# Performance work log

Measured on AMD Instinct MI355X. Metric: run time of the kernel, lower is better.

Reference implementation:

```python
import jax, jax.numpy as jnp
import numpy as np

N = 50000      # nodes
E = 800000     # edges (before self-loops)
IN_CH = 5
HID = 32
HEADS = 4
NEG_SLOPE = 0.2  # PyG GATConv default


def _gat_layer(x, src, dst, W, att_src, att_dst, bias, concat):
    """PyG GATConv (eval mode). W: [F_in, H*C], att_*: [H, C], bias matches output."""
    H, C = att_src.shape
    h = (x @ W).reshape(-1, H, C)                       # [N, H, C]
    a_src = jnp.sum(h * att_src, axis=-1)               # [N, H]
    a_dst = jnp.sum(h * att_dst, axis=-1)               # [N, H]
    e = jax.nn.leaky_relu(a_src[src] + a_dst[dst], negative_slope=NEG_SLOPE)  # [E', H]
    m = jax.ops.segment_max(e, dst, num_segments=N)     # stable softmax per dst segment
    ex = jnp.exp(e - m[dst])
    denom = jax.ops.segment_sum(ex, dst, num_segments=N)
    alpha = ex / denom[dst]                             # [E', H]
    out = jax.ops.segment_sum(alpha[:, :, None] * h[src], dst, num_segments=N)  # [N, H, C]
    out = out.reshape(N, H * C) if concat else out.mean(axis=1)
    return out + bias


def setup_inputs() -> dict:
    key = jax.random.key(0)
    ks = jax.random.split(key, 14)
    g = lambda k, shape, s=0.1: (jax.random.normal(k, shape, jnp.float32) * s)
    return {
        "x": jax.random.normal(ks[0], (N, IN_CH), jnp.float32),
        "edge_index": jax.random.randint(ks[1], (2, E), 0, N, jnp.int32),
        "W1": g(ks[2], (IN_CH, HEADS * HID)),
        "att_src1": g(ks[3], (HEADS, HID)),
        "att_dst1": g(ks[4], (HEADS, HID)),
        "b1": jnp.zeros((HEADS * HID,), jnp.float32),
        "W2": g(ks[5], (HEADS * HID, HID)),
        "att_src2": g(ks[6], (1, HID)),
        "att_dst2": g(ks[7], (1, HID)),
        "b2": jnp.zeros((HID,), jnp.float32),
        "Wc1": g(ks[8], (HID, 16)),
        "bc1": jnp.zeros((16,), jnp.float32),
        "Wc2": g(ks[9], (16, 1)),
        "bc2": jnp.zeros((1,), jnp.float32),
    }


def reference(x, edge_index, W1, att_src1, att_dst1, b1, W2, att_src2, att_dst2, b2, Wc1, bc1, Wc2, bc2):
    # add self loops (PyG GATConv default add_self_loops=True)
    loops = jnp.arange(N, dtype=edge_index.dtype)
    src = jnp.concatenate([edge_index[0], loops])
    dst = jnp.concatenate([edge_index[1], loops])
    # dropout layers are identity in eval mode
    h = jax.nn.elu(_gat_layer(x, src, dst, W1, att_src1, att_dst1, b1, concat=True))
    h = jax.nn.elu(_gat_layer(h, src, dst, W2, att_src2, att_dst2, b2, concat=False))
    h = jax.nn.relu(h @ Wc1 + bc1)
    out = (h @ Wc2 + bc2)[:, 0]   # squeeze(-1) -> [N]
    return out
```

## Files before the change

kernel.cpp:

```cpp
#include <hip/hip_runtime.h>
#include <hip/hip_fp16.h>

#define NEG_SLOPE 0.2f
#define BSHIFT 6
#define SCATB 256

__device__ __forceinline__ float elu1(float v) { return v > 0.f ? v : expm1f(v); }
__device__ __forceinline__ float lrelu(float v) { return v > 0.f ? v : NEG_SLOPE * v; }

__device__ __forceinline__ int ge_off(const int* __restrict__ blkoff,
                                      const int* __restrict__ bsum2, int j) {
    if (j == 0) return 0;
    int b = (j - 1) >> 8;
    int v = blkoff[j];
    if (b >= 1) v += bsum2[b - 1];
    return v;
}


__global__ __launch_bounds__(256) void k_cnt_attn(
    const int* __restrict__ ei, int E, int ET, int chunk,
    int* __restrict__ Cmat, int nbuck,
    const float* __restrict__ x, const float* __restrict__ W1,
    const float* __restrict__ att_s, const float* __restrict__ att_d,
    float* __restrict__ rec, int N) {
    __shared__ int hist[784];
    __shared__ float Ps[5][4], Pd[5][4];
    if (blockIdx.x < SCATB) {
        for (int i = threadIdx.x; i < nbuck; i += 256) hist[i] = 0;
        __syncthreads();
        int k = blockIdx.x;
        int e0 = k * chunk, e1 = min(e0 + chunk, ET);
        for (int e = e0 + threadIdx.x; e < e1; e += 256) {
            int d = (e < E) ? ei[E + e] : e - E;
            atomicAdd(&hist[d >> BSHIFT], 1);
        }
        __syncthreads();
        for (int i = threadIdx.x; i < nbuck; i += 256)
            Cmat[i * SCATB + k] = hist[i];
    } else {
        if (threadIdx.x < 40) {
            int pair = threadIdx.x & 1, idx = threadIdx.x >> 1;
            int k = idx >> 2, h = idx & 3;
            const float* att = pair ? att_d : att_s;
            float r = 0.f;
#pragma unroll
            for (int c = 0; c < 32; ++c) r = fmaf(W1[k * 128 + h * 32 + c], att[h * 32 + c], r);
            if (pair) Pd[k][h] = r; else Ps[k][h] = r;
        }
        __syncthreads();
        int n = (blockIdx.x - SCATB) * 256 + threadIdx.x;
        if (n >= N) return;
        float xv[5];
#pragma unroll
        for (int k = 0; k < 5; ++k) xv[k] = x[(size_t)n * 5 + k];
        float s0 = 0, s1 = 0, s2 = 0, s3 = 0, d0 = 0, d1 = 0, d2 = 0, d3 = 0;
#pragma unroll
        for (int k = 0; k < 5; ++k) {
            s0 = fmaf(xv[k], Ps[k][0], s0); s1 = fmaf(xv[k], Ps[k][1], s1);
            s2 = fmaf(xv[k], Ps[k][2], s2); s3 = fmaf(xv[k], Ps[k][3], s3);
            d0 = fmaf(xv[k], Pd[k][0], d0); d1 = fmaf(xv[k], Pd[k][1], d1);
            d2 = fmaf(xv[k], Pd[k][2], d2); d3 = fmaf(xv[k], Pd[k][3], d3);
        }
        float* r = rec + (size_t)n * 16;
        *(float4*)(r)      = make_float4(s0, s1, s2, s3);
        *(float4*)(r + 4)  = make_float4(xv[0], xv[1], xv[2], xv[3]);
        r[8] = xv[4];
        *(float4*)(r + 12) = make_float4(d0, d1, d2, d3);
    }
}

__global__ __launch_bounds__(256) void k_scan1(
    const int* __restrict__ Cmat, int* __restrict__ blkoff, int* __restrict__ bsum, int M) {
    __shared__ int ws4[4], wsoff[4];
    int i = blockIdx.x * 256 + threadIdx.x;
    int lane = threadIdx.x & 63, w = threadIdx.x >> 6;
    int v = (i < M) ? Cmat[i] : 0;
    int sc = v;
#pragma unroll
    for (int m = 1; m < 64; m <<= 1) {
        int t = __shfl_up(sc, m, 64);
        if (lane >= m) sc += t;
    }
    if (lane == 63) ws4[w] = sc;
    __syncthreads();
    if (threadIdx.x == 0) {
        int r = 0;
#pragma unroll
        for (int j = 0; j < 4; ++j) { wsoff[j] = r; r += ws4[j]; }
        bsum[blockIdx.x] = r;
    }
    __syncthreads();
    if (i < M) blkoff[i + 1] = sc + wsoff[w];
}

__global__ __launch_bounds__(1024) void k_scan2(
    int* __restrict__ bsum, int nb, int* __restrict__ off, int N, int ET) {
    __shared__ int wsum[16];
    int i = threadIdx.x, lane = i & 63, w = i >> 6;
    if (i == 0) off[N] = ET;
    int v = (i < nb) ? bsum[i] : 0, sc = v;
#pragma unroll
    for (int m = 1; m < 64; m <<= 1) {
        int t = __shfl_up(sc, m, 64);
        if (lane >= m) sc += t;
    }
    if (lane == 63) wsum[w] = sc;
    __syncthreads();
    if (w == 0 && lane < 16) {
        int s2 = wsum[lane];
#pragma unroll
        for (int m = 1; m < 16; m <<= 1) {
            int t = __shfl_up(s2, m, 16);
            if (lane >= m) s2 += t;
        }
        wsum[lane] = s2;
    }
    __syncthreads();
    int carry = (w == 0) ? 0 : wsum[w - 1];
    if (i < nb) bsum[i] = carry + sc;
}

__global__ __launch_bounds__(256) void k_scat(
    const int* __restrict__ ei, int E, int ET, int chunk,
    const int* __restrict__ blkoff, const int* __restrict__ bsum2,
    unsigned* __restrict__ pairs, int nbuck) {
    __shared__ int cur[784];
    int k = blockIdx.x;
    for (int i = threadIdx.x; i < nbuck; i += 256)
        cur[i] = ge_off(blkoff, bsum2, i * SCATB + k);
    __syncthreads();
    int e0 = k * chunk, e1 = min(e0 + chunk, ET);
    for (int e = e0 + threadIdx.x; e < e1; e += 256) {
        int s, d;
        if (e < E) { s = ei[e]; d = ei[E + e]; } else { s = d = e - E; }
        int p = atomicAdd(&cur[d >> BSHIFT], 1);
        pairs[p] = (unsigned)s | ((unsigned)(d & 63) << 16);
    }
}

__global__ __launch_bounds__(256) void k_sortB(
    const unsigned* __restrict__ pairs, const int* __restrict__ blkoff,
    const int* __restrict__ bsum2, int* __restrict__ off,
    int* __restrict__ csr_src, int N, int ET, int nbuck) {
    __shared__ int hist[64], cur[64];
    __shared__ unsigned pl[1536];
    int b = blockIdx.x;
    int base = ge_off(blkoff, bsum2, b * SCATB);
    int end  = (b + 1 < nbuck) ? ge_off(blkoff, bsum2, (b + 1) * SCATB) : ET;
    int cnt = end - base;
    int stg = min(cnt, 1536);
    int dstBase = b << BSHIFT;
    if (threadIdx.x < 64) hist[threadIdx.x] = 0;
    for (int i = threadIdx.x; i < stg; i += 256) pl[i] = pairs[base + i];
    __syncthreads();
    for (int i = threadIdx.x; i < cnt; i += 256) {
        unsigned pr = (i < stg) ? pl[i] : pairs[base + i];
        atomicAdd(&hist[pr >> 16], 1);
    }
    __syncthreads();
    if (threadIdx.x < 64) {
        int v = hist[threadIdx.x], sc = v;
#pragma unroll
        for (int m = 1; m < 64; m <<= 1) {
            int t = __shfl_up(sc, m, 64);
            if (threadIdx.x >= m) sc += t;
        }
        int ex = sc - v;
        cur[threadIdx.x] = ex;
        int d = dstBase + threadIdx.x;
        if (d < N) off[d] = base + ex;
    }
    __syncthreads();
    for (int i = threadIdx.x; i < cnt; i += 256) {
        unsigned pr = (i < stg) ? pl[i] : pairs[base + i];
        int r = atomicAdd(&cur[pr >> 16], 1);
        csr_src[base + r] = (int)(pr & 0xFFFFu);
    }
}


__global__ __launch_bounds__(256) void k_agg1(
    const int* __restrict__ off, const int* __restrict__ csr_src,
    const float* __restrict__ rec, const float* __restrict__ W1,
    const float* __restrict__ b1, __half* __restrict__ out1h, int N) {
    __shared__ float Wl[5 * 128];
    __shared__ float b1l[128];
    for (int i = threadIdx.x; i < 5 * 128; i += 256) Wl[i] = W1[i];
    if (threadIdx.x < 128) b1l[threadIdx.x] = b1[threadIdx.x];
    __syncthreads();
    int g = (blockIdx.x * 256 + threadIdx.x) >> 4;
    int lane = threadIdx.x & 15;
    if (g >= N) return;
    int p0 = off[g], p1 = off[g + 1];
    float4 ad = *(const float4*)(rec + (size_t)g * 16 + 12);
    float den0 = 0, den1 = 0, den2 = 0, den3 = 0;
    float acc[4][5] = {};
    for (int p = p0 + lane; p < p1; p += 16) {
        int s = csr_src[p];
        const float* r = rec + (size_t)s * 16;
        float4 as  = *(const float4*)r;
        float4 x03 = *(const float4*)(r + 4);
        float  x4  = r[8];
        float v0 = __expf(lrelu(as.x + ad.x));
        float v1 = __expf(lrelu(as.y + ad.y));
        float v2 = __expf(lrelu(as.z + ad.z));
        float v3 = __expf(lrelu(as.w + ad.w));
        den0 += v0; den1 += v1; den2 += v2; den3 += v3;
        float xk[5] = {x03.x, x03.y, x03.z, x03.w, x4};
#pragma unroll
        for (int k = 0; k < 5; ++k) {
            acc[0][k] = fmaf(v0, xk[k], acc[0][k]);
            acc[1][k] = fmaf(v1, xk[k], acc[1][k]);
            acc[2][k] = fmaf(v2, xk[k], acc[2][k]);
            acc[3][k] = fmaf(v3, xk[k], acc[3][k]);
        }
    }
#pragma unroll
    for (int m = 8; m; m >>= 1) {
        den0 += __shfl_xor(den0, m, 16); den1 += __shfl_xor(den1, m, 16);
        den2 += __shfl_xor(den2, m, 16); den3 += __shfl_xor(den3, m, 16);
#pragma unroll
        for (int h = 0; h < 4; ++h)
#pragma unroll
            for (int k = 0; k < 5; ++k) acc[h][k] += __shfl_xor(acc[h][k], m, 16);
    }
    int c0 = lane * 8;
    int h = lane >> 2;
    float dh = (h == 0) ? den0 : (h == 1) ? den1 : (h == 2) ? den2 : den3;
    float ih = 1.f / dh;
    float ag[5];
#pragma unroll
    for (int k = 0; k < 5; ++k) ag[k] = acc[h][k] * ih;
    __half2 ph[4];
#pragma unroll
    for (int j = 0; j < 4; ++j) {
        int c = c0 + 2 * j;
        float rr = b1l[c];
#pragma unroll
        for (int k = 0; k < 5; ++k) rr = fmaf(ag[k], Wl[k * 128 + c], rr);
        float oa = elu1(rr);
        rr = b1l[c + 1];
#pragma unroll
        for (int k = 0; k < 5; ++k) rr = fmaf(ag[k], Wl[k * 128 + c + 1], rr);
        float ob = elu1(rr);
        ph[j] = __floats2half2_rn(oa, ob);
    }
    *(float4*)(out1h + (size_t)g * 128 + c0) = *(float4*)ph;
}


__global__ __launch_bounds__(256) void k_feat2(
    const __half* __restrict__ out1h, const float* __restrict__ W2,
    const float* __restrict__ att_s, const float* __restrict__ att_d,
    __half* __restrict__ h2h, float* __restrict__ a_s, float* __restrict__ a_d, int N) {
    __shared__ float Wl[128 * 32];
    for (int i = threadIdx.x; i < 128 * 32; i += 256) Wl[i] = W2[i];
    __syncthreads();
    int t = blockIdx.x * 256 + threadIdx.x;
    int n = t >> 5, c = t & 31;
    if (n >= N) return;
    const float4* hr4 = (const float4*)(out1h + (size_t)n * 128);
    float acc = 0.f;
#pragma unroll
    for (int k4 = 0; k4 < 16; ++k4) {
        float4 q = hr4[k4];
        const __half2* hp = (const __half2*)&q;
#pragma unroll
        for (int m = 0; m < 4; ++m) {
            float2 f = __half22float2(hp[m]);
            acc = fmaf(f.x, Wl[(k4 * 8 + 2 * m) * 32 + c], acc);
            acc = fmaf(f.y, Wl[(k4 * 8 + 2 * m + 1) * 32 + c], acc);
        }
    }
    h2h[(size_t)n * 32 + c] = __float2half_rn(acc);
    float as = acc * att_s[c], ad = acc * att_d[c];
#pragma unroll
    for (int m = 16; m; m >>= 1) {
        as += __shfl_xor(as, m, 32);
        ad += __shfl_xor(ad, m, 32);
    }
    if (c == 0) { a_s[n] = as; a_d[n] = ad; }
}

__global__ __launch_bounds__(256) void k_agg2h(
    const int* __restrict__ off, const int* __restrict__ csr_src,
    const float* __restrict__ a_s, const float* __restrict__ a_d,
    const __half* __restrict__ h2h, const float* __restrict__ b2,
    const float* __restrict__ Wc1, const float* __restrict__ bc1,
    const float* __restrict__ Wc2, const float* __restrict__ bc2,
    float* __restrict__ out, int N) {
    __shared__ float Wl[512];
    __shared__ float b2l[32], b1l[16], w2l[16];
    for (int i = threadIdx.x; i < 512; i += 256) Wl[i] = Wc1[i];
    if (threadIdx.x < 32) b2l[threadIdx.x] = b2[threadIdx.x];
    if (threadIdx.x < 16) {
        b1l[threadIdx.x] = bc1[threadIdx.x];
        w2l[threadIdx.x] = Wc2[threadIdx.x];
    }
    __syncthreads();
    int g = (blockIdx.x * 256 + threadIdx.x) >> 5;
    int lane = threadIdx.x & 31;
    if (g >= N) return;
    int p0 = off[g], p1 = off[g + 1];
    float ad = a_d[g];
    float acc = 0.f, den = 0.f;
    for (int base = p0; base < p1; base += 32) {
        int rem = p1 - base;
        int s = g;
        float w = 0.f;
        if (lane < rem) {
            s = csr_src[base + lane];
            w = __expf(lrelu(a_s[s] + ad));
        }
        den += w;
        int cnt = min(rem, 32);
        int rc = (cnt + 7) & ~7;
        for (int j = 0; j < rc; j += 8) {
#pragma unroll
            for (int jj = 0; jj < 8; ++jj) {
                int   sj = __shfl(s, j + jj, 32);
                float wj = __shfl(w, j + jj, 32);
                float hv = __half2float(h2h[(size_t)sj * 32 + lane]);
                acc = fmaf(wj, hv, acc);
            }
        }
    }
#pragma unroll
    for (int m = 16; m; m >>= 1) den += __shfl_xor(den, m, 32);
    float z = elu1(fmaf(acc, 1.f / den, b2l[lane]));
    float y = b1l[lane & 15];
#pragma unroll
    for (int c = 0; c < 32; ++c) {
        float zc = __shfl(z, c, 32);
        y = fmaf(zc, Wl[c * 16 + (lane & 15)], y);
    }
    y = fmaxf(y, 0.f);
    float t = (lane < 16) ? y * w2l[lane] : 0.f;
#pragma unroll
    for (int m = 8; m; m >>= 1) t += __shfl_xor(t, m, 32);
    if (lane == 0) out[g] = t + bc2[0];
}

extern "C" void kernel_launch(void* const* d_in, const int* in_sizes, int n_in,
                              void* d_out, int out_size, void* d_ws, size_t ws_size,
                              hipStream_t stream) {
    const float* x   = (const float*)d_in[0];
    const int*   ei  = (const int*)d_in[1];
    const float* W1  = (const float*)d_in[2];
    const float* as1 = (const float*)d_in[3];
    const float* ad1 = (const float*)d_in[4];
    const float* b1  = (const float*)d_in[5];
    const float* W2  = (const float*)d_in[6];
    const float* as2 = (const float*)d_in[7];
    const float* ad2 = (const float*)d_in[8];
    const float* b2  = (const float*)d_in[9];
    const float* Wc1 = (const float*)d_in[10];
    const float* bc1 = (const float*)d_in[11];
    const float* Wc2 = (const float*)d_in[12];
    const float* bc2 = (const float*)d_in[13];
    float* out = (float*)d_out;

    const int N = out_size;
    const int E = in_sizes[1] / 2;
    const int ET = E + N;
    const int nbuck = (N + 63) >> BSHIFT;
    const int M = nbuck * SCATB;
    const int chunk = (ET + SCATB - 1) / SCATB;

    float*    ws    = (float*)d_ws;
    __half*   out1h = (__half*)ws;
    __half*   h2h   = (__half*)(ws + (size_t)N * 64);
    float*    rec   = ws + (size_t)N * 80;
    float*    a_s2  = rec  + (size_t)N * 16;
    float*    a_d2  = a_s2 + N;
    int*      off   = (int*)(a_d2 + N);
    int*      csr_src = off + (N + 2);
    int*      Cmat  = csr_src + ET;
    int*      blkoff = Cmat + M;
    int*      bsum  = blkoff + (M + 2);
    unsigned* pairs = (unsigned*)(bsum + 1024);

    auto cdiv = [](long long a, long long b) { return (int)((a + b - 1) / b); };
    const int B = 256;
    const int NB2 = cdiv(M, B);
    const int nAttn = cdiv(N, B);

    k_cnt_attn<<<SCATB + nAttn, B, 0, stream>>>(ei, E, ET, chunk, Cmat, nbuck,
                                                x, W1, as1, ad1, rec, N);
    k_scan1<<<NB2, B, 0, stream>>>(Cmat, blkoff, bsum, M);
    k_scan2<<<1, 1024, 0, stream>>>(bsum, NB2, off, N, ET);
    k_scat<<<SCATB, B, 0, stream>>>(ei, E, ET, chunk, blkoff, bsum, pairs, nbuck);
    k_sortB<<<nbuck, B, 0, stream>>>(pairs, blkoff, bsum, off, csr_src, N, ET, nbuck);

    k_agg1<<<cdiv((long long)N * 16, B), B, 0, stream>>>(off, csr_src, rec, W1, b1, out1h, N);

    k_feat2<<<cdiv((long long)N * 32, B), B, 0, stream>>>(out1h, W2, as2, ad2, h2h, a_s2, a_d2, N);
    k_agg2h<<<cdiv((long long)N * 32, B), B, 0, stream>>>(off, csr_src, a_s2, a_d2, h2h, b2,
                                                          Wc1, bc1, Wc2, bc2, out, N);
}
```

Baseline: 117.6 us.

## Single-pass decoupled-lookback scan, fp16 node records, transposed fp16 W2 in LDS

Replaces the two-kernel scan (block scan plus a single-block carry scan) with one decoupled-lookback scan that uses a ticket counter and per-block descriptors. The descriptors are zeroed inside the first kernel, which also makes blkoff fully global so consumers no longer add the carry. Layer-1 node records are packed as fp16 (32 B) and a_dst is moved to a separate float4 array, cutting gather bytes in agg1. k_feat2 stores W2 transposed in fp16 in LDS so each thread reads contiguous half2 weights. These changes trade one launch for spin-wait risk and add fp16 rounding of the attention logits and input features.

```diff
diff --git a/kernel.cpp b/kernel.cpp
--- a/kernel.cpp
+++ b/kernel.cpp
@@ -7,15 +7,6 @@
 
 __device__ __forceinline__ float elu1(float v) { return v > 0.f ? v : expm1f(v); }
 __device__ __forceinline__ float lrelu(float v) { return v > 0.f ? v : NEG_SLOPE * v; }
-
-__device__ __forceinline__ int ge_off(const int* __restrict__ blkoff,
-                                      const int* __restrict__ bsum2, int j) {
-    if (j == 0) return 0;
-    int b = (j - 1) >> 8;
-    int v = blkoff[j];
-    if (b >= 1) v += bsum2[b - 1];
-    return v;
-}
 
 
 __global__ __launch_bounds__(256) void k_cnt_attn(
@@ -23,7 +14,8 @@
     int* __restrict__ Cmat, int nbuck,
     const float* __restrict__ x, const float* __restrict__ W1,
     const float* __restrict__ att_s, const float* __restrict__ att_d,
-    float* __restrict__ rec, int N) {
+    __half* __restrict__ rech, float4* __restrict__ ad4f, int N,
+    int nAttn, int* __restrict__ dzero, int nzero) {
     __shared__ int hist[784];
     __shared__ float Ps[5][4], Pd[5][4];
     if (blockIdx.x < SCATB) {
@@ -38,7 +30,7 @@
         __syncthreads();
         for (int i = threadIdx.x; i < nbuck; i += 256)
             Cmat[i * SCATB + k] = hist[i];
-    } else {
+    } else if (blockIdx.x < SCATB + nAttn) {
         if (threadIdx.x < 40) {
             int pair = threadIdx.x & 1, idx = threadIdx.x >> 1;
             int k = idx >> 2, h = idx & 3;
@@ -62,18 +54,32 @@
             d0 = fmaf(xv[k], Pd[k][0], d0); d1 = fmaf(xv[k], Pd[k][1], d1);
             d2 = fmaf(xv[k], Pd[k][2], d2); d3 = fmaf(xv[k], Pd[k][3], d3);
         }
-        float* r = rec + (size_t)n * 16;
-        *(float4*)(r)      = make_float4(s0, s1, s2, s3);
-        *(float4*)(r + 4)  = make_float4(xv[0], xv[1], xv[2], xv[3]);
-        r[8] = xv[4];
-        *(float4*)(r + 12) = make_float4(d0, d1, d2, d3);
-    }
-}
-
-__global__ __launch_bounds__(256) void k_scan1(
-    const int* __restrict__ Cmat, int* __restrict__ blkoff, int* __restrict__ bsum, int M) {
+        __half2 a[4], b[4];
+        a[0] = __floats2half2_rn(s0, s1);
+        a[1] = __floats2half2_rn(s2, s3);
+        a[2] = __floats2half2_rn(xv[0], xv[1]);
+        a[3] = __floats2half2_rn(xv[2], xv[3]);
+        b[0] = __floats2half2_rn(xv[4], 0.f);
+        b[1] = b[2] = b[3] = __floats2half2_rn(0.f, 0.f);
+        *(float4*)(rech + (size_t)n * 16)     = *(float4*)a;
+        *(float4*)(rech + (size_t)n * 16 + 8) = *(float4*)b;
+        ad4f[n] = make_float4(d0, d1, d2, d3);
+    } else {
+        int i = (blockIdx.x - SCATB - nAttn) * 256 + threadIdx.x;
+        if (i < nzero) dzero[i] = 0;
+    }
+}
+
+__global__ __launch_bounds__(256) void k_scanL(
+    const int* __restrict__ Cmat, int* __restrict__ blkoff,
+    unsigned long long* __restrict__ desc, int* __restrict__ ticket,
+    int M, int* __restrict__ off, int N, int ET) {
+    __shared__ int sbid, sprefix, stot;
     __shared__ int ws4[4], wsoff[4];
-    int i = blockIdx.x * 256 + threadIdx.x;
+    if (threadIdx.x == 0) sbid = atomicAdd(ticket, 1);
+    __syncthreads();
+    int bid = sbid;
+    int i = bid * 256 + threadIdx.x;
     int lane = threadIdx.x & 63, w = threadIdx.x >> 6;
     int v = (i < M) ? Cmat[i] : 0;
     int sc = v;
@@ -88,47 +94,60 @@
         int r = 0;
 #pragma unroll
         for (int j = 0; j < 4; ++j) { wsoff[j] = r; r += ws4[j]; }
-        bsum[blockIdx.x] = r;
-    }
-    __syncthreads();
-    if (i < M) blkoff[i + 1] = sc + wsoff[w];
-}
-
-__global__ __launch_bounds__(1024) void k_scan2(
-    int* __restrict__ bsum, int nb, int* __restrict__ off, int N, int ET) {
-    __shared__ int wsum[16];
-    int i = threadIdx.x, lane = i & 63, w = i >> 6;
-    if (i == 0) off[N] = ET;
-    int v = (i < nb) ? bsum[i] : 0, sc = v;
-#pragma unroll
-    for (int m = 1; m < 64; m <<= 1) {
-        int t = __shfl_up(sc, m, 64);
-        if (lane >= m) sc += t;
-    }
-    if (lane == 63) wsum[w] = sc;
-    __syncthreads();
-    if (w == 0 && lane < 16) {
-        int s2 = wsum[lane];
-#pragma unroll
-        for (int m = 1; m < 16; m <<= 1) {
-            int t = __shfl_up(s2, m, 16);
-            if (lane >= m) s2 += t;
-        }
-        wsum[lane] = s2;
-    }
-    __syncthreads();
-    int carry = (w == 0) ? 0 : wsum[w - 1];
-    if (i < nb) bsum[i] = carry + sc;
+        stot = r;
+        unsigned long long d = ((unsigned long long)((bid == 0) ? 2u : 1u) << 32) | (unsigned)r;
+        __hip_atomic_store(&desc[bid], d, __ATOMIC_RELEASE, __HIP_MEMORY_SCOPE_AGENT);
+        if (bid == 0) sprefix = 0;
+    }
+    __syncthreads();
+    if (bid > 0 && w == 0) {
+        int running = 0;
+        int end = bid;
+        while (true) {
+            int w0 = end - 64; if (w0 < 0) w0 = 0;
+            int idx = w0 + lane;
+            bool valid = idx < end;
+            int st, val;
+            do {
+                unsigned long long d = valid
+                    ? __hip_atomic_load(&desc[idx], __ATOMIC_ACQUIRE, __HIP_MEMORY_SCOPE_AGENT)
+                    : (2ULL << 32);
+                st = (int)(d >> 32);
+                val = (int)(d & 0xffffffffULL);
+            } while (__any(st == 0));
+            unsigned long long m2 = __ballot(valid && st == 2);
+            int contrib;
+            if (m2) {
+                int hbit = 63 - __clzll(m2);
+                contrib = (valid && lane >= hbit) ? val : 0;
+            } else {
+                contrib = valid ? val : 0;
+            }
+#pragma unroll
+            for (int mm = 32; mm; mm >>= 1) contrib += __shfl_xor(contrib, mm, 64);
+            running += contrib;
+            if (m2) break;
+            end = w0;
+        }
+        if (lane == 0) {
+            sprefix = running;
+            unsigned long long d = (2ULL << 32) | (unsigned)(running + stot);
+            __hip_atomic_store(&desc[bid], d, __ATOMIC_RELEASE, __HIP_MEMORY_SCOPE_AGENT);
+        }
+    }
+    __syncthreads();
+    int ex = sprefix;
+    if (i < M) blkoff[i + 1] = ex + sc + wsoff[w];
+    if (i == 0) { blkoff[0] = 0; off[N] = ET; }
 }
 
 __global__ __launch_bounds__(256) void k_scat(
     const int* __restrict__ ei, int E, int ET, int chunk,
-    const int* __restrict__ blkoff, const int* __restrict__ bsum2,
-    unsigned* __restrict__ pairs, int nbuck) {
+    const int* __restrict__ blkoff, unsigned* __restrict__ pairs, int nbuck) {
     __shared__ int cur[784];
     int k = blockIdx.x;
     for (int i = threadIdx.x; i < nbuck; i += 256)
-        cur[i] = ge_off(blkoff, bsum2, i * SCATB + k);
+        cur[i] = blkoff[i * SCATB + k];
     __syncthreads();
     int e0 = k * chunk, e1 = min(e0 + chunk, ET);
     for (int e = e0 + threadIdx.x; e < e1; e += 256) {
@@ -141,13 +160,12 @@
 
 __global__ __launch_bounds__(256) void k_sortB(
     const unsigned* __restrict__ pairs, const int* __restrict__ blkoff,
-    const int* __restrict__ bsum2, int* __restrict__ off,
-    int* __restrict__ csr_src, int N, int ET, int nbuck) {
+    int* __restrict__ off, int* __restrict__ csr_src, int N, int nbuck) {
     __shared__ int hist[64], cur[64];
     __shared__ unsigned pl[1536];
     int b = blockIdx.x;
-    int base = ge_off(blkoff, bsum2, b * SCATB);
-    int end  = (b + 1 < nbuck) ? ge_off(blkoff, bsum2, (b + 1) * SCATB) : ET;
+    int base = blkoff[b * SCATB];
+    int end  = blkoff[(b + 1) * SCATB];
     int cnt = end - base;
     int stg = min(cnt, 1536);
     int dstBase = b << BSHIFT;
@@ -182,8 +200,9 @@
 
 __global__ __launch_bounds__(256) void k_agg1(
     const int* __restrict__ off, const int* __restrict__ csr_src,
-    const float* __restrict__ rec, const float* __restrict__ W1,
-    const float* __restrict__ b1, __half* __restrict__ out1h, int N) {
+    const __half* __restrict__ rech, const float4* __restrict__ ad4f,
+    const float* __restrict__ W1, const float* __restrict__ b1,
+    __half* __restrict__ out1h, int N) {
     __shared__ float Wl[5 * 128];
     __shared__ float b1l[128];
     for (int i = threadIdx.x; i < 5 * 128; i += 256) Wl[i] = W1[i];
@@ -193,21 +212,25 @@
     int lane = threadIdx.x & 15;
     if (g >= N) return;
     int p0 = off[g], p1 = off[g + 1];
-    float4 ad = *(const float4*)(rec + (size_t)g * 16 + 12);
+    float4 ad = ad4f[g];
     float den0 = 0, den1 = 0, den2 = 0, den3 = 0;
     float acc[4][5] = {};
     for (int p = p0 + lane; p < p1; p += 16) {
         int s = csr_src[p];
-        const float* r = rec + (size_t)s * 16;
-        float4 as  = *(const float4*)r;
-        float4 x03 = *(const float4*)(r + 4);
-        float  x4  = r[8];
-        float v0 = __expf(lrelu(as.x + ad.x));
-        float v1 = __expf(lrelu(as.y + ad.y));
-        float v2 = __expf(lrelu(as.z + ad.z));
-        float v3 = __expf(lrelu(as.w + ad.w));
+        const __half* r = rech + (size_t)s * 16;
+        float4 q = *(const float4*)r;
+        const __half2* hp = (const __half2*)&q;
+        float2 as01 = __half22float2(hp[0]);
+        float2 as23 = __half22float2(hp[1]);
+        float2 x01  = __half22float2(hp[2]);
+        float2 x23  = __half22float2(hp[3]);
+        float  x4   = __half2float(r[8]);
+        float v0 = __expf(lrelu(as01.x + ad.x));
+        float v1 = __expf(lrelu(as01.y + ad.y));
+        float v2 = __expf(lrelu(as23.x + ad.z));
+        float v3 = __expf(lrelu(as23.y + ad.w));
         den0 += v0; den1 += v1; den2 += v2; den3 += v3;
-        float xk[5] = {x03.x, x03.y, x03.z, x03.w, x4};
+        float xk[5] = {x01.x, x01.y, x23.x, x23.y, x4};
 #pragma unroll
         for (int k = 0; k < 5; ++k) {
             acc[0][k] = fmaf(v0, xk[k], acc[0][k]);
@@ -254,13 +277,17 @@
     const __half* __restrict__ out1h, const float* __restrict__ W2,
     const float* __restrict__ att_s, const float* __restrict__ att_d,
     __half* __restrict__ h2h, float* __restrict__ a_s, float* __restrict__ a_d, int N) {
-    __shared__ float Wl[128 * 32];
-    for (int i = threadIdx.x; i < 128 * 32; i += 256) Wl[i] = W2[i];
+    __shared__ __half Wt[32 * 132];
+    for (int i = threadIdx.x; i < 4096; i += 256) {
+        int k = i >> 5, c = i & 31;
+        Wt[c * 132 + k] = __float2half_rn(W2[i]);
+    }
     __syncthreads();
     int t = blockIdx.x * 256 + threadIdx.x;
     int n = t >> 5, c = t & 31;
     if (n >= N) return;
     const float4* hr4 = (const float4*)(out1h + (size_t)n * 128);
+    const __half2* wrow = (const __half2*)(Wt + c * 132);
     float acc = 0.f;
 #pragma unroll
     for (int k4 = 0; k4 < 16; ++k4) {
@@ -268,9 +295,10 @@
         const __half2* hp = (const __half2*)&q;
 #pragma unroll
         for (int m = 0; m < 4; ++m) {
-            float2 f = __half22float2(hp[m]);
-            acc = fmaf(f.x, Wl[(k4 * 8 + 2 * m) * 32 + c], acc);
-            acc = fmaf(f.y, Wl[(k4 * 8 + 2 * m + 1) * 32 + c], acc);
+            float2 f  = __half22float2(hp[m]);
+            float2 wv = __half22float2(wrow[k4 * 4 + m]);
+            acc = fmaf(f.x, wv.x, acc);
+            acc = fmaf(f.y, wv.y, acc);
         }
     }
     h2h[(size_t)n * 32 + c] = __float2half_rn(acc);
@@ -368,34 +396,41 @@
     const int M = nbuck * SCATB;
     const int chunk = (ET + SCATB - 1) / SCATB;
 
+    auto cdiv = [](long long a, long long b) { return (int)((a + b - 1) / b); };
+    const int B = 256;
+    const int nBlk = cdiv(M, B);
+    const int nAttn = cdiv(N, B);
+
     float*    ws    = (float*)d_ws;
     __half*   out1h = (__half*)ws;
     __half*   h2h   = (__half*)(ws + (size_t)N * 64);
-    float*    rec   = ws + (size_t)N * 80;
-    float*    a_s2  = rec  + (size_t)N * 16;
+    __half*   rech  = (__half*)(ws + (size_t)N * 80);
+    float4*   ad4f  = (float4*)(ws + (size_t)N * 88);
+    float*    a_s2  = ws + (size_t)N * 92;
     float*    a_d2  = a_s2 + N;
     int*      off   = (int*)(a_d2 + N);
     int*      csr_src = off + (N + 2);
     int*      Cmat  = csr_src + ET;
     int*      blkoff = Cmat + M;
-    int*      bsum  = blkoff + (M + 2);
-    unsigned* pairs = (unsigned*)(bsum + 1024);
-
-    auto cdiv = [](long long a, long long b) { return (int)((a + b - 1) / b); };
-    const int B = 256;
-    const int NB2 = cdiv(M, B);
-    const int nAttn = cdiv(N, B);
-
-    k_cnt_attn<<<SCATB + nAttn, B, 0, stream>>>(ei, E, ET, chunk, Cmat, nbuck,
-                                                x, W1, as1, ad1, rec, N);
-    k_scan1<<<NB2, B, 0, stream>>>(Cmat, blkoff, bsum, M);
-    k_scan2<<<1, 1024, 0, stream>>>(bsum, NB2, off, N, ET);
-    k_scat<<<SCATB, B, 0, stream>>>(ei, E, ET, chunk, blkoff, bsum, pairs, nbuck);
-    k_sortB<<<nbuck, B, 0, stream>>>(pairs, blkoff, bsum, off, csr_src, N, ET, nbuck);
-
-    k_agg1<<<cdiv((long long)N * 16, B), B, 0, stream>>>(off, csr_src, rec, W1, b1, out1h, N);
-
-    k_feat2<<<cdiv((long long)N * 32, B), B, 0, stream>>>(out1h, W2, as2, ad2, h2h, a_s2, a_d2, N);
+    size_t    daddr = ((size_t)(blkoff + M + 2) + 7) & ~(size_t)7;
+    unsigned long long* desc = (unsigned long long*)daddr;
+    int*      ticket = (int*)(desc + nBlk);
+    unsigned* pairs = (unsigned*)(ticket + 4);
+    const int nzero = 2 * nBlk + 4;
+    const int nZeroBlk = cdiv(nzero, B);
+
+    k_cnt_attn<<<SCATB + nAttn + nZeroBlk, B, 0, stream>>>(
+        ei, E, ET, chunk, Cmat, nbuck, x, W1, as1, ad1, rech, ad4f, N,
+        nAttn, (int*)desc, nzero);
+    k_scanL<<<nBlk, B, 0, stream>>>(Cmat, blkoff, desc, ticket, M, off, N, ET);
+    k_scat<<<SCATB, B, 0, stream>>>(ei, E, ET, chunk, blkoff, pairs, nbuck);
+    k_sortB<<<nbuck, B, 0, stream>>>(pairs, blkoff, off, csr_src, N, nbuck);
+
+    k_agg1<<<cdiv((long long)N * 16, B), B, 0, stream>>>(off, csr_src, rech, ad4f,
+                                                         W1, b1, out1h, N);
+
+    k_feat2<<<cdiv((long long)N * 32, B), B, 0, stream>>>(out1h, W2, as2, ad2, h2h,
+                                                          a_s2, a_d2, N);
     k_agg2h<<<cdiv((long long)N * 32, B), B, 0, stream>>>(off, csr_src, a_s2, a_d2, h2h, b2,
                                                           Wc1, bc1, Wc2, bc2, out, N);
 }
```

After: 167.0 us. 42.0% more time.
